# Performance work log

Measured on AMD Instinct MI355X. Metric: run time of the kernel, lower is better.

The kernel has to match this reference:

```python
import jax, jax.numpy as jnp
import numpy as np

# 8 directional difference stencils (N, S, E, W, NE, SE, SW, NW), OIHW [8,1,3,3]
_WINDOWS = np.array([
    [[0, 1, 0], [0, -1, 0], [0, 0, 0]],
    [[0, 0, 0], [0, -1, 0], [0, 1, 0]],
    [[0, 0, 0], [0, -1, 1], [0, 0, 0]],
    [[0, 0, 0], [1, -1, 0], [0, 0, 0]],
    [[0, 0, 1], [0, -1, 0], [0, 0, 0]],
    [[0, 0, 0], [0, -1, 0], [0, 0, 1]],
    [[0, 0, 0], [0, -1, 0], [1, 0, 0]],
    [[1, 0, 0], [0, -1, 0], [0, 0, 0]],
], dtype=np.float32).reshape(8, 1, 3, 3)

ITERATIONS = 30  # int(self.iterations.item()) with init value 30.0


def setup_inputs() -> dict:
    key = jax.random.key(0)
    k1, k2, k3 = jax.random.split(key, 3)
    x = jax.random.normal(k1, (32, 3, 512, 512), dtype=jnp.float32)
    W_expand = jax.random.normal(k2, (3, 3, 1, 1), dtype=jnp.float32) * 0.3
    b_expand = jax.random.normal(k3, (3,), dtype=jnp.float32) * 0.1
    return {
        "x": x,
        "delta": jnp.float32(0.1),
        "kappa": jnp.float32(15.0),
        "W_expand": W_expand,
        "b_expand": b_expand,
    }


def reference(x, delta, kappa, W_expand, b_expand):
    K = jnp.asarray(_WINDOWS)  # [8,1,3,3]
    # axial directions weight 1, diagonal directions weight 1/(sqrt(2))^2 = 0.5
    dir_w = jnp.array([1.0, 1.0, 1.0, 1.0, 0.5, 0.5, 0.5, 0.5],
                      dtype=x.dtype).reshape(1, 8, 1, 1)

    # RGB -> luminance, [B,1,H,W]
    u = (0.299 * x[:, 0] + 0.587 * x[:, 1] + 0.114 * x[:, 2])[:, None]

    def step(u, _):
        # all 8 directional gradients in one grouped conv: [B,8,H,W]
        nabla = jax.lax.conv_general_dilated(
            u, K, window_strides=(1, 1), padding='SAME',
            dimension_numbers=('NCHW', 'OIHW', 'NCHW'))
        diff = 1.0 / (1.0 + (nabla / kappa) ** 2)  # Perona-Malik diffusivity
        upd = jnp.sum(dir_w * diff * nabla, axis=1, keepdims=True)
        return u + delta * upd, None

    u, _ = jax.lax.scan(step, u, None, length=ITERATIONS)

    # repeat to 3 channels then 1x1 conv (expand_channels)
    u_rgb = jnp.repeat(u, 3, axis=1)  # [B,3,H,W]
    out = jnp.einsum('oi,bihw->bohw', W_expand[:, :, 0, 0], u_rgb)
    out = out + b_expand[None, :, None, None]
    return out
```

## Files before the change

kernel.cpp:

```cpp
#include <hip/hip_runtime.h>

#define BATCH 32
#define HGT 512
#define WID 512
#define PLANE (HGT * WID)
#define NPIX (BATCH * PLANE)
#define BSTRIDE (3 * PLANE)
#define NQUAD (NPIX / 4)

#define RSLAB 32
#define SLABS (HGT / RSLAB)
#define FBLOCKS (BATCH * SLABS)
#define FT 512

__device__ __forceinline__ float4 ld4(const float* p) {
    return *reinterpret_cast<const float4*>(p);
}
__device__ __forceinline__ void st4(float* p, float4 v) {
    *reinterpret_cast<float4*>(p) = v;
}

__device__ __forceinline__ float pm_flux(float d, float ik2) {
    return d * __builtin_amdgcn_rcpf(fmaf(d * d, ik2, 1.f));
}

__device__ __forceinline__ int swz(int q) {
    return ((q & 1) << 8) + ((q >> 1) << 2);
}

__device__ __forceinline__ void load_row10(const float* __restrict__ buf, int row, int o,
                                           float m[10]) {
    const float* p = buf + row * WID + (o << 2);
    float4 lo = ld4(p);
    float4 hi = ld4(p + 256);
    float le = __shfl_up(hi.w, 1);
    float re = __shfl_down(lo.x, 1);
    m[0] = (o == 0) ? 0.f : le;
    m[1] = lo.x; m[2] = lo.y; m[3] = lo.z; m[4] = lo.w;
    m[5] = hi.x; m[6] = hi.y; m[7] = hi.z; m[8] = hi.w;
    m[9] = (o == 63) ? 0.f : re;
}

template <int MODE, int S>
__global__ __launch_bounds__(FT, 4)
void pm_fusedk(const float* __restrict__ src, int sstr,
               float* __restrict__ dst, int dstr,
               const float* __restrict__ pdelta, const float* __restrict__ pkappa,
               const float* __restrict__ Wexp, const float* __restrict__ bexp) {
    constexpr int LR = RSLAB + 2 * S;
    __shared__ float buf[LR * WID];

    const int img  = blockIdx.x >> 4;
    const int slab = blockIdx.x & (SLABS - 1);
    const int H0   = slab * RSLAB;
    const int tid  = threadIdx.x;
    const int wave = tid >> 6;
    const int o    = tid & 63;

    const float delta = *pdelta;
    const float kappa = *pkappa;
    const float ik2 = __builtin_amdgcn_rcpf(kappa * kappa);

    const float* sb = src + (size_t)img * sstr;
    for (int i = tid; i < LR * (WID / 4); i += FT) {
        int row = i >> 7;
        int q   = i & 127;
        int g = H0 - S + row;
        float4 v = make_float4(0.f, 0.f, 0.f, 0.f);
        if ((unsigned)g < (unsigned)HGT) {
            const float* p = sb + g * WID + (q << 2);
            if (MODE == 0) {
                float4 r = ld4(p), gg = ld4(p + PLANE), bb = ld4(p + 2 * PLANE);
                v.x = fmaf(0.299f, r.x, fmaf(0.587f, gg.x, 0.114f * bb.x));
                v.y = fmaf(0.299f, r.y, fmaf(0.587f, gg.y, 0.114f * bb.y));
                v.z = fmaf(0.299f, r.z, fmaf(0.587f, gg.z, 0.114f * bb.z));
                v.w = fmaf(0.299f, r.w, fmaf(0.587f, gg.w, 0.114f * bb.w));
            } else {
                v = ld4(p);
            }
        }
        int dsto = (MODE == 0) ? swz(q) : (q << 2);
        st4(buf + row * WID + dsto, v);
    }
    __syncthreads();

    float s0c = 0.f, s1c = 0.f, s2c = 0.f, b0c = 0.f, b1c = 0.f, b2c = 0.f;
    if (MODE == 2) {
        s0c = Wexp[0] + Wexp[1] + Wexp[2];
        s1c = Wexp[3] + Wexp[4] + Wexp[5];
        s2c = Wexp[6] + Wexp[7] + Wexp[8];
        b0c = bexp[0]; b1c = bexp[1]; b2c = bexp[2];
    }

    float* db = dst + (size_t)img * dstr;

    for (int s = 0; s < S; ++s) {
        const int tot = LR - 2 - 2 * s;
        const int bse = tot >> 3, rem = tot & 7;
        const int n   = bse + (wave < rem ? 1 : 0);
        const int st0 = s + 1 + wave * bse + (wave < rem ? wave : rem);
        const bool fin = (s == S - 1);

        float a[10], m[10], d[10];
        load_row10(buf, st0 - 1, o, a);
        load_row10(buf, st0, o, m);

        float f8[8], l8[8], rp[8];

        for (int i = 0; i < n; ++i) {
            load_row10(buf, st0 + i + 1, o, d);

            float hF[9];
#pragma unroll
            for (int t = 0; t < 9; ++t) hF[t] = pm_flux(m[t + 1] - m[t], ik2);

            float o8[8];
#pragma unroll
            for (int j = 0; j < 8; ++j) {
                float c = m[j + 1];
                float ax = hF[j + 1] - hF[j];
                ax += pm_flux(a[j + 1] - c, ik2);
                ax += pm_flux(d[j + 1] - c, ik2);
                float dg = pm_flux(a[j] - c, ik2);
                dg += pm_flux(a[j + 2] - c, ik2);
                dg += pm_flux(d[j] - c, ik2);
                dg += pm_flux(d[j + 2] - c, ik2);
                o8[j] = fmaf(delta, fmaf(0.5f, dg, ax), c);
            }

            const int g = H0 - S + st0 + i;
            if ((unsigned)g >= (unsigned)HGT) {
#pragma unroll
                for (int j = 0; j < 8; ++j) o8[j] = 0.f;
            }

            if (fin) {
                if (MODE == 2) {
                    float* p = db + (size_t)g * WID + (o << 3);
                    st4(p, make_float4(fmaf(s0c, o8[0], b0c), fmaf(s0c, o8[1], b0c),
                                       fmaf(s0c, o8[2], b0c), fmaf(s0c, o8[3], b0c)));
                    st4(p + 4, make_float4(fmaf(s0c, o8[4], b0c), fmaf(s0c, o8[5], b0c),
                                           fmaf(s0c, o8[6], b0c), fmaf(s0c, o8[7], b0c)));
                    st4(p + PLANE,
                        make_float4(fmaf(s1c, o8[0], b1c), fmaf(s1c, o8[1], b1c),
                                    fmaf(s1c, o8[2], b1c), fmaf(s1c, o8[3], b1c)));
                    st4(p + PLANE + 4,
                        make_float4(fmaf(s1c, o8[4], b1c), fmaf(s1c, o8[5], b1c),
                                    fmaf(s1c, o8[6], b1c), fmaf(s1c, o8[7], b1c)));
                    st4(p + 2 * PLANE,
                        make_float4(fmaf(s2c, o8[0], b2c), fmaf(s2c, o8[1], b2c),
                                    fmaf(s2c, o8[2], b2c), fmaf(s2c, o8[3], b2c)));
                    st4(p + 2 * PLANE + 4,
                        make_float4(fmaf(s2c, o8[4], b2c), fmaf(s2c, o8[5], b2c),
                                    fmaf(s2c, o8[6], b2c), fmaf(s2c, o8[7], b2c)));
                } else {
                    float* p = db + (size_t)g * WID + (o << 2);
                    st4(p, make_float4(o8[0], o8[1], o8[2], o8[3]));
                    st4(p + 256, make_float4(o8[4], o8[5], o8[6], o8[7]));
                }
            } else if (i == 0) {
#pragma unroll
                for (int j = 0; j < 8; ++j) f8[j] = o8[j];
            } else {
                if (i >= 2) {
                    float* p = buf + (st0 + i - 1) * WID + (o << 2);
                    st4(p, make_float4(rp[0], rp[1], rp[2], rp[3]));
                    st4(p + 256, make_float4(rp[4], rp[5], rp[6], rp[7]));
                }
                if (i == n - 1) {
#pragma unroll
                    for (int j = 0; j < 8; ++j) l8[j] = o8[j];
                } else {
#pragma unroll
                    for (int j = 0; j < 8; ++j) rp[j] = o8[j];
                }
            }

#pragma unroll
            for (int t = 0; t < 10; ++t) { a[t] = m[t]; m[t] = d[t]; }
        }

        if (!fin) {
            __syncthreads();
            float* p = buf + st0 * WID + (o << 2);
            st4(p, make_float4(f8[0], f8[1], f8[2], f8[3]));
            st4(p + 256, make_float4(f8[4], f8[5], f8[6], f8[7]));
            p = buf + (st0 + n - 1) * WID + (o << 2);
            st4(p, make_float4(l8[0], l8[1], l8[2], l8[3]));
            st4(p + 256, make_float4(l8[4], l8[5], l8[6], l8[7]));
            __syncthreads();
        }
    }
}

__global__ void expand_from(const float* __restrict__ usrc, int ustr,
                            float* __restrict__ out,
                            const float* __restrict__ Wexp,
                            const float* __restrict__ bexp) {
    int idx = blockIdx.x * blockDim.x + threadIdx.x;
    if (idx >= NQUAD) return;
    int b = idx / (PLANE / 4);
    int pq = idx - b * (PLANE / 4);
    int row = pq >> 7;
    int q   = pq & 127;

    float4 u = ld4(usrc + (size_t)b * ustr + row * WID + swz(q));
    float s0 = Wexp[0] + Wexp[1] + Wexp[2];
    float s1 = Wexp[3] + Wexp[4] + Wexp[5];
    float s2 = Wexp[6] + Wexp[7] + Wexp[8];
    float b0 = bexp[0], b1 = bexp[1], b2 = bexp[2];

    size_t base = (size_t)b * BSTRIDE + row * WID + (q << 2);
    st4(out + base, make_float4(fmaf(s0, u.x, b0), fmaf(s0, u.y, b0),
                                fmaf(s0, u.z, b0), fmaf(s0, u.w, b0)));
    st4(out + base + PLANE, make_float4(fmaf(s1, u.x, b1), fmaf(s1, u.y, b1),
                                        fmaf(s1, u.z, b1), fmaf(s1, u.w, b1)));
    st4(out + base + 2 * PLANE, make_float4(fmaf(s2, u.x, b2), fmaf(s2, u.y, b2),
                                            fmaf(s2, u.z, b2), fmaf(s2, u.w, b2)));
}

extern "C" void kernel_launch(void* const* d_in, const int* in_sizes, int n_in,
                              void* d_out, int out_size, void* d_ws, size_t ws_size,
                              hipStream_t stream) {
    const float* x      = (const float*)d_in[0];
    const float* pdelta = (const float*)d_in[1];
    const float* pkappa = (const float*)d_in[2];
    const float* Wexp   = (const float*)d_in[3];
    const float* bexp   = (const float*)d_in[4];
    float* out = (float*)d_out;

    const size_t need = (size_t)2 * NPIX * sizeof(float);
    if (ws_size >= need) {
        float* uA = (float*)d_ws;
        float* uB = uA + NPIX;
        pm_fusedk<0, 4><<<FBLOCKS, FT, 0, stream>>>(
            x, BSTRIDE, uA, PLANE, pdelta, pkappa, Wexp, bexp);
        float* s = uA;
        float* d = uB;
        for (int k = 0; k < 6; ++k) {
            pm_fusedk<1, 4><<<FBLOCKS, FT, 0, stream>>>(
                s, PLANE, d, PLANE, pdelta, pkappa, Wexp, bexp);
            float* t = s; s = d; d = t;
        }
        pm_fusedk<2, 2><<<FBLOCKS, FT, 0, stream>>>(
            s, PLANE, out, BSTRIDE, pdelta, pkappa, Wexp, bexp);
    } else {
        float* uA = out;
        float* uB = out + PLANE;
        pm_fusedk<0, 4><<<FBLOCKS, FT, 0, stream>>>(
            x, BSTRIDE, uA, BSTRIDE, pdelta, pkappa, Wexp, bexp);
        float* s = uA;
        float* d = uB;
        for (int k = 0; k < 6; ++k) {
            pm_fusedk<1, 4><<<FBLOCKS, FT, 0, stream>>>(
                s, BSTRIDE, d, BSTRIDE, pdelta, pkappa, Wexp, bexp);
            float* t = s; s = d; d = t;
        }
        pm_fusedk<1, 2><<<FBLOCKS, FT, 0, stream>>>(
            s, BSTRIDE, d, BSTRIDE, pdelta, pkappa, Wexp, bexp);
        const int block = 256;
        const int grid_q = (NQUAD + block - 1) / block;
        expand_from<<<grid_q, block, 0, stream>>>(d, BSTRIDE, out, Wexp, bexp);
    }
}
```

Before: 442.4 us.

## Reuse antisymmetric vertical and diagonal fluxes across consecutive rows

Uses the antisymmetry of the pairwise Perona-Malik flux. Vertical and diagonal fluxes between each pair of adjacent rows are computed once, kept in a register state and reused by both rows, which cuts the per-row flux evaluations from 57 to 35. The flux is also rewritten to use kappa² directly, dropping one multiply per evaluation. The row loop is unrolled by two to ping-pong between two register states, and interior rows are written back to LDS right away instead of through a delayed copy. The extra live registers may cause spills or lower occupancy under the 512-thread, 4-blocks-per-CU launch bound.

```diff
diff --git a/kernel.cpp b/kernel.cpp
--- a/kernel.cpp
+++ b/kernel.cpp
@@ -20,8 +20,8 @@
     *reinterpret_cast<float4*>(p) = v;
 }
 
-__device__ __forceinline__ float pm_flux(float d, float ik2) {
-    return d * __builtin_amdgcn_rcpf(fmaf(d * d, ik2, 1.f));
+__device__ __forceinline__ float pm_flux(float d, float k2) {
+    return (k2 * d) * __builtin_amdgcn_rcpf(fmaf(d, d, k2));
 }
 
 __device__ __forceinline__ int swz(int q) {
@@ -41,6 +41,22 @@
     m[9] = (o == 63) ? 0.f : re;
 }
 
+struct FluxState {
+    float m[10];
+    float pV[8], pSE[9], pSW[9];
+};
+
+__device__ __forceinline__ void level10(const float a[10], const float b[10],
+                                        float vF[8], float seF[9], float swF[9],
+                                        float k2) {
+#pragma unroll
+    for (int j = 0; j < 8; ++j) vF[j] = pm_flux(b[j + 1] - a[j + 1], k2);
+#pragma unroll
+    for (int i = 0; i < 9; ++i) seF[i] = pm_flux(b[i + 1] - a[i], k2);
+#pragma unroll
+    for (int i = 0; i < 9; ++i) swF[i] = pm_flux(b[i] - a[i + 1], k2);
+}
+
 template <int MODE, int S>
 __global__ __launch_bounds__(FT, 4)
 void pm_fusedk(const float* __restrict__ src, int sstr,
@@ -59,7 +75,7 @@
 
     const float delta = *pdelta;
     const float kappa = *pkappa;
-    const float ik2 = __builtin_amdgcn_rcpf(kappa * kappa);
+    const float k2 = kappa * kappa;
 
     const float* sb = src + (size_t)img * sstr;
     for (int i = tid; i < LR * (WID / 4); i += FT) {
@@ -101,39 +117,34 @@
         const int st0 = s + 1 + wave * bse + (wave < rem ? wave : rem);
         const bool fin = (s == S - 1);
 
-        float a[10], m[10], d[10];
-        load_row10(buf, st0 - 1, o, a);
-        load_row10(buf, st0, o, m);
-
-        float f8[8], l8[8], rp[8];
-
-        for (int i = 0; i < n; ++i) {
-            load_row10(buf, st0 + i + 1, o, d);
-
+        FluxState A, B;
+        {
+            float a10[10];
+            load_row10(buf, st0 - 1, o, a10);
+            load_row10(buf, st0, o, A.m);
+            level10(a10, A.m, A.pV, A.pSE, A.pSW, k2);
+        }
+        float f8[8], l8[8];
+
+        auto do_row = [&](FluxState& CUR, FluxState& NXT, int i) {
+            load_row10(buf, st0 + i + 1, o, NXT.m);
             float hF[9];
 #pragma unroll
-            for (int t = 0; t < 9; ++t) hF[t] = pm_flux(m[t + 1] - m[t], ik2);
-
+            for (int t = 0; t < 9; ++t) hF[t] = pm_flux(CUR.m[t + 1] - CUR.m[t], k2);
+            level10(CUR.m, NXT.m, NXT.pV, NXT.pSE, NXT.pSW, k2);
             float o8[8];
 #pragma unroll
             for (int j = 0; j < 8; ++j) {
-                float c = m[j + 1];
-                float ax = hF[j + 1] - hF[j];
-                ax += pm_flux(a[j + 1] - c, ik2);
-                ax += pm_flux(d[j + 1] - c, ik2);
-                float dg = pm_flux(a[j] - c, ik2);
-                dg += pm_flux(a[j + 2] - c, ik2);
-                dg += pm_flux(d[j] - c, ik2);
-                dg += pm_flux(d[j + 2] - c, ik2);
-                o8[j] = fmaf(delta, fmaf(0.5f, dg, ax), c);
-            }
-
+                float ax = NXT.pV[j] - CUR.pV[j] + hF[j + 1] - hF[j];
+                float dg = NXT.pSE[j + 1] + NXT.pSW[j]
+                         - CUR.pSE[j] - CUR.pSW[j + 1];
+                o8[j] = fmaf(delta, fmaf(0.5f, dg, ax), CUR.m[j + 1]);
+            }
             const int g = H0 - S + st0 + i;
             if ((unsigned)g >= (unsigned)HGT) {
 #pragma unroll
                 for (int j = 0; j < 8; ++j) o8[j] = 0.f;
             }
-
             if (fin) {
                 if (MODE == 2) {
                     float* p = db + (size_t)g * WID + (o << 3);
@@ -161,23 +172,19 @@
             } else if (i == 0) {
 #pragma unroll
                 for (int j = 0; j < 8; ++j) f8[j] = o8[j];
+            } else if (i == n - 1) {
+#pragma unroll
+                for (int j = 0; j < 8; ++j) l8[j] = o8[j];
             } else {
-                if (i >= 2) {
-                    float* p = buf + (st0 + i - 1) * WID + (o << 2);
-                    st4(p, make_float4(rp[0], rp[1], rp[2], rp[3]));
-                    st4(p + 256, make_float4(rp[4], rp[5], rp[6], rp[7]));
-                }
-                if (i == n - 1) {
-#pragma unroll
-                    for (int j = 0; j < 8; ++j) l8[j] = o8[j];
-                } else {
-#pragma unroll
-                    for (int j = 0; j < 8; ++j) rp[j] = o8[j];
-                }
-            }
-
-#pragma unroll
-            for (int t = 0; t < 10; ++t) { a[t] = m[t]; m[t] = d[t]; }
+                float* p = buf + (st0 + i) * WID + (o << 2);
+                st4(p, make_float4(o8[0], o8[1], o8[2], o8[3]));
+                st4(p + 256, make_float4(o8[4], o8[5], o8[6], o8[7]));
+            }
+        };
+
+        for (int i = 0; i < n; i += 2) {
+            do_row(A, B, i);
+            if (i + 1 < n) do_row(B, A, i + 1);
         }
 
         if (!fin) {
```

New measurement: 404.7 us. -8.5%, faster.
